# Optimization experiments

Measured on AMD Instinct MI355X. Metric: run time of the kernel, lower is better.

Reference implementation:

```python
import jax, jax.numpy as jnp
import numpy as np

KE_KCAL = 332.0637  # Coulomb constant in kcal/mol * Angstrom / e^2
R_CUT = 10.0
R_ON = R_CUT / 4.0
R_OFF = 3.0 * R_CUT / 4.0
MAX_Z = 86
FEAT_DIM = 128
N_ATOMS = 6144


def sigma(x):
    # torch.where(x > 0, exp(-1/x), 0) -- guard the exp arg so no NaN under jit
    xs = jnp.where(x > 0, x, 1.0)
    return jnp.where(x > 0, jnp.exp(-1.0 / xs), 0.0)


def f_switch(r):
    arg = (r - R_ON) / (R_OFF - R_ON)
    s_up = sigma(1.0 - arg)
    s_dn = sigma(arg)
    return s_up / (s_up + s_dn)


def setup_inputs() -> dict:
    key = jax.random.key(0)
    k_f, k_z, k_x, k_w, k_t = jax.random.split(key, 5)
    f = jax.random.normal(k_f, (N_ATOMS, FEAT_DIM), dtype=jnp.float32)
    z = jax.random.randint(k_z, (N_ATOMS,), 0, MAX_Z, dtype=jnp.int64)
    xyz = jax.random.uniform(k_x, (N_ATOMS, 3), dtype=jnp.float32) * 60.0  # ~60 A box
    total_charge = jnp.zeros((1,), dtype=jnp.float32)
    # learned params: Dense(feat_dim -> 1, no bias) and Embedding(max_z, 1) with padding row 0
    w_weight = jax.random.normal(k_w, (1, FEAT_DIM), dtype=jnp.float32) * 0.05
    z_table = jax.random.normal(k_t, (MAX_Z, 1), dtype=jnp.float32) * 0.05
    z_table = z_table.at[0].set(0.0)  # padding_idx=0
    return {"f": f, "z": z, "xyz": xyz, "total_charge": total_charge,
            "w_weight": w_weight, "z_table": z_table}


def reference(f, z, xyz, total_charge, w_weight, z_table):
    n = f.shape[0]
    # --- get_charge ---
    pred_charge = f @ w_weight.T + z_table[z]          # [N, 1]
    correction = (total_charge[0] - pred_charge.sum()) / n
    q = pred_charge + correction                       # [N, 1]
    qv = q[:, 0]                                       # [N]
    # --- get_en: pairwise distances via gram trick (no [N,N,3] intermediate) ---
    sq = jnp.sum(xyz * xyz, axis=-1)                   # [N]
    r2 = sq[:, None] + sq[None, :] - 2.0 * (xyz @ xyz.T)
    r2 = jnp.maximum(r2, 0.0)                          # [N, N]
    iu = jnp.triu(jnp.ones((n, n), dtype=bool), k=1)
    mask = iu & (r2 > 0.0)                             # j > i and r > 0, as in the torch code
    r2_safe = jnp.where(mask, r2, 1.0)
    r = jnp.sqrt(r2_safe)
    fs = f_switch(r)
    term = fs / jnp.sqrt(r2_safe + 1.0) + (1.0 - fs) / r
    pair_e = jnp.where(mask, qv[:, None] * qv[None, :] * term, 0.0)
    energy = KE_KCAL * jnp.sum(pair_e)
    return energy, q
```

## Files before the change

kernel.cpp:

```cpp
#include <hip/hip_runtime.h>

#define KE_KCAL 332.0637f

constexpr int N_ATOMS = 6144;
constexpr int NREAL = 1200;
constexpr int NPRED = 384;
constexpr int PAD = 32;

__global__ __launch_bounds__(256) void pred_kernel(
    const float* __restrict__ f, const int* __restrict__ z,
    const float* __restrict__ w, const float* __restrict__ ztab,
    const float* __restrict__ xyz,
    float* __restrict__ qpart, float4* __restrict__ xqp,
    float* __restrict__ epart, unsigned int* __restrict__ ctr1,
    unsigned int* __restrict__ ctr2)
{
    int t = threadIdx.x, b = blockIdx.x;
    int lane = t & 63, wid = t >> 6;

    if (b == 0) {
        if (t < 64) { epart[t * PAD] = 0.f; ctr1[t * PAD] = 0u; }
        if (t == 64) *ctr2 = 0u;
    }

    int base = b * 16 + wid * 4;
    const float2* f2 = (const float2*)f;
    float2 wv = ((const float2*)w)[lane];
    float2 v0 = f2[(size_t)(base + 0) * 64 + lane];
    float2 v1 = f2[(size_t)(base + 1) * 64 + lane];
    float2 v2 = f2[(size_t)(base + 2) * 64 + lane];
    float2 v3 = f2[(size_t)(base + 3) * 64 + lane];
    float p0 = fmaf(v0.x, wv.x, v0.y * wv.y);
    float p1 = fmaf(v1.x, wv.x, v1.y * wv.y);
    float p2 = fmaf(v2.x, wv.x, v2.y * wv.y);
    float p3 = fmaf(v3.x, wv.x, v3.y * wv.y);
    #pragma unroll
    for (int off = 32; off > 0; off >>= 1) {
        p0 += __shfl_xor(p0, off, 64);
        p1 += __shfl_xor(p1, off, 64);
        p2 += __shfl_xor(p2, off, 64);
        p3 += __shfl_xor(p3, off, 64);
    }
    float ws_sum = 0.f;
    if (lane < 4) {
        int atom = base + lane;
        float pk = p0;
        pk = (lane == 1) ? p1 : pk;
        pk = (lane == 2) ? p2 : pk;
        pk = (lane == 3) ? p3 : pk;
        pk += ztab[z[atom]];
        xqp[atom] = make_float4(xyz[3*atom], xyz[3*atom+1], xyz[3*atom+2], pk);
        ws_sum = pk;
    }
    ws_sum += __shfl_xor(ws_sum, 1, 64);
    ws_sum += __shfl_xor(ws_sum, 2, 64);

    __shared__ float lred[4];
    if (lane == 0) lred[wid] = ws_sum;
    __syncthreads();
    if (t == 0) qpart[b] = lred[0] + lred[1] + lred[2] + lred[3];
}

__global__ __launch_bounds__(256) void pair_kernel(
    const float4* __restrict__ xqp, const float* __restrict__ qpart,
    const float* __restrict__ total_charge,
    float* __restrict__ qout, float* __restrict__ epart,
    unsigned int* __restrict__ ctr1, unsigned int* __restrict__ ctr2,
    float* __restrict__ out0)
{
    int t = threadIdx.x, b = blockIdx.x;
    int lane = t & 63, wid = t >> 6;
    __shared__ float lred[4];
    __shared__ float4 sj[64];

    float s = qpart[t];
    if (t < NPRED - 256) s += qpart[256 + t];
    #pragma unroll
    for (int off = 32; off > 0; off >>= 1)
        s += __shfl_xor(s, off, 64);
    if (lane == 0) lred[wid] = s;
    __syncthreads();
    float S = lred[0] + lred[1] + lred[2] + lred[3];
    float corr = (total_charge[0] - S) * (1.0f / (float)N_ATOMS);

    int bi = 0, off = 0;
    while (b >= off + (96 - 4 * bi)) { off += 96 - 4 * bi; ++bi; }
    int bj = 4 * bi + (b - off);

    int gj0 = bj * 64;
    if (t < 64) {
        float4 a = xqp[gj0 + t];
        a.w += corr;
        sj[t] = a;
    }
    int gi = bi * 256 + t;
    float4 pi = xqp[gi];
    float qi = pi.w + corr;
    if (bj == 4 * bi) qout[gi] = qi;
    __syncthreads();

    int jthresh = gi - gj0;
    float acc = 0.f;
    #pragma unroll 8
    for (int jj = 0; jj < 64; ++jj) {
        float4 pj = sj[jj];
        float dx = pi.x - pj.x, dy = pi.y - pj.y, dz = pi.z - pj.z;
        float r2 = fmaf(dx, dx, fmaf(dy, dy, dz * dz));
        bool m = (jj > jthresh) && (r2 > 0.f);
        float r2s = m ? r2 : 1e8f;
        float qq  = m ? qi * pj.w : 0.f;
        float t2  = __builtin_amdgcn_rsqf(r2s);
        float u   = fmaf(r2s * t2, 0.2f, -0.5f);
        u = fminf(fmaxf(u, 1e-3f), 0.999f);
        float d   = (u + u - 1.f) * __builtin_amdgcn_rcpf(fmaf(-u, u, u));
        float fs  = __builtin_amdgcn_rcpf(1.f + __expf(d));
        float t1  = __builtin_amdgcn_rsqf(r2s + 1.f);
        acc = fmaf(qq, fmaf(fs, t1 - t2, t2), acc);
    }

    #pragma unroll
    for (int o2 = 32; o2 > 0; o2 >>= 1)
        acc += __shfl_down(acc, o2, 64);
    __syncthreads();
    if (lane == 0) lred[wid] = acc;
    __syncthreads();
    if (t == 0) {
        float be = lred[0] + lred[1] + lred[2] + lred[3];
        atomicAdd(&epart[(b & 63) * PAD], be);
    }

    if (t < 64) {
        bool last = false;
        if (t == 0) {
            int g = b & 63;
            unsigned int gcnt = (g < 48) ? 19u : 18u;
            __threadfence();
            unsigned int o1 = atomicAdd(&ctr1[g * PAD], 1u);
            if (o1 == gcnt - 1u) {
                __threadfence();
                unsigned int o2c = atomicAdd(ctr2, 1u);
                last = (o2c == 63u);
            }
        }
        last = (bool)__shfl((int)last, 0, 64);
        if (last) {
            float e = atomicAdd(&epart[t * PAD], 0.0f);
            #pragma unroll
            for (int o2 = 32; o2 > 0; o2 >>= 1)
                e += __shfl_down(e, o2, 64);
            if (t == 0) out0[0] = KE_KCAL * e;
        }
    }
}

extern "C" void kernel_launch(void* const* d_in, const int* in_sizes, int n_in,
                              void* d_out, int out_size, void* d_ws, size_t ws_size,
                              hipStream_t stream) {
    const float* f    = (const float*)d_in[0];
    const int*   z    = (const int*)  d_in[1];
    const float* xyz  = (const float*)d_in[2];
    const float* qtot = (const float*)d_in[3];
    const float* w    = (const float*)d_in[4];
    const float* ztab = (const float*)d_in[5];
    float* out = (float*)d_out;

    char* wsb = (char*)d_ws;
    float*        epart = (float*)(wsb + 0);
    unsigned int* ctr1  = (unsigned int*)(wsb + 8192);
    unsigned int* ctr2  = (unsigned int*)(wsb + 16384);
    float*        qpart = (float*)(wsb + 16896);
    float4*       xqp   = (float4*)(wsb + 32768);

    pred_kernel<<<NPRED, 256, 0, stream>>>(f, z, w, ztab, xyz,
                                           qpart, xqp, epart, ctr1, ctr2);
    pair_kernel<<<NREAL, 256, 0, stream>>>(xqp, qpart, qtot, out + 1, epart,
                                           ctr1, ctr2, out);
}
```

Measured before the change: 92.90 us.

## Fuse charge prediction and pair energy into one kernel with flag-based grid sync

Merges the per-atom charge prediction and the pairwise energy kernels into a single launch. The first NPRED blocks compute charges, and the last of them to finish reduces the partial sums and publishes the charge correction through a release flag. Every block spin-waits on that flag before doing its pair tile. The final energy reduction now writes one partial per block and lets the last block sum them, replacing the float atomics on padded slots. A tiny init kernel zeroes the counters, the pair loop unroll drops from 8 to 4, and the kernel gets an occupancy hint. The spin-wait relies on all blocks being co-resident and on the cross-block memory ordering being correct.

```diff
diff --git a/kernel.cpp b/kernel.cpp
--- a/kernel.cpp
+++ b/kernel.cpp
@@ -7,81 +7,103 @@
 constexpr int NPRED = 384;
 constexpr int PAD = 32;
 
-__global__ __launch_bounds__(256) void pred_kernel(
+
+__global__ __launch_bounds__(64) void init_kernel(unsigned int* __restrict__ c)
+{
+    for (int k = threadIdx.x; k < 2112; k += 64) c[k] = 0u;
+}
+
+__global__ __launch_bounds__(256, 8) void mega_kernel(
     const float* __restrict__ f, const int* __restrict__ z,
     const float* __restrict__ w, const float* __restrict__ ztab,
-    const float* __restrict__ xyz,
-    float* __restrict__ qpart, float4* __restrict__ xqp,
-    float* __restrict__ epart, unsigned int* __restrict__ ctr1,
-    unsigned int* __restrict__ ctr2)
-{
-    int t = threadIdx.x, b = blockIdx.x;
-    int lane = t & 63, wid = t >> 6;
-
-    if (b == 0) {
-        if (t < 64) { epart[t * PAD] = 0.f; ctr1[t * PAD] = 0u; }
-        if (t == 64) *ctr2 = 0u;
-    }
-
-    int base = b * 16 + wid * 4;
-    const float2* f2 = (const float2*)f;
-    float2 wv = ((const float2*)w)[lane];
-    float2 v0 = f2[(size_t)(base + 0) * 64 + lane];
-    float2 v1 = f2[(size_t)(base + 1) * 64 + lane];
-    float2 v2 = f2[(size_t)(base + 2) * 64 + lane];
-    float2 v3 = f2[(size_t)(base + 3) * 64 + lane];
-    float p0 = fmaf(v0.x, wv.x, v0.y * wv.y);
-    float p1 = fmaf(v1.x, wv.x, v1.y * wv.y);
-    float p2 = fmaf(v2.x, wv.x, v2.y * wv.y);
-    float p3 = fmaf(v3.x, wv.x, v3.y * wv.y);
-    #pragma unroll
-    for (int off = 32; off > 0; off >>= 1) {
-        p0 += __shfl_xor(p0, off, 64);
-        p1 += __shfl_xor(p1, off, 64);
-        p2 += __shfl_xor(p2, off, 64);
-        p3 += __shfl_xor(p3, off, 64);
-    }
-    float ws_sum = 0.f;
-    if (lane < 4) {
-        int atom = base + lane;
-        float pk = p0;
-        pk = (lane == 1) ? p1 : pk;
-        pk = (lane == 2) ? p2 : pk;
-        pk = (lane == 3) ? p3 : pk;
-        pk += ztab[z[atom]];
-        xqp[atom] = make_float4(xyz[3*atom], xyz[3*atom+1], xyz[3*atom+2], pk);
-        ws_sum = pk;
-    }
-    ws_sum += __shfl_xor(ws_sum, 1, 64);
-    ws_sum += __shfl_xor(ws_sum, 2, 64);
-
-    __shared__ float lred[4];
-    if (lane == 0) lred[wid] = ws_sum;
-    __syncthreads();
-    if (t == 0) qpart[b] = lred[0] + lred[1] + lred[2] + lred[3];
-}
-
-__global__ __launch_bounds__(256) void pair_kernel(
-    const float4* __restrict__ xqp, const float* __restrict__ qpart,
-    const float* __restrict__ total_charge,
-    float* __restrict__ qout, float* __restrict__ epart,
+    const float* __restrict__ xyz, const float* __restrict__ qtot,
+    float* __restrict__ qout, float* __restrict__ out0,
     unsigned int* __restrict__ ctr1, unsigned int* __restrict__ ctr2,
-    float* __restrict__ out0)
+    unsigned int* __restrict__ pred_ctr, unsigned int* __restrict__ flag,
+    float* __restrict__ cslot, float* __restrict__ qpart,
+    float* __restrict__ eblk, float4* __restrict__ xqp)
 {
     int t = threadIdx.x, b = blockIdx.x;
     int lane = t & 63, wid = t >> 6;
     __shared__ float lred[4];
     __shared__ float4 sj[64];
-
-    float s = qpart[t];
-    if (t < NPRED - 256) s += qpart[256 + t];
-    #pragma unroll
-    for (int off = 32; off > 0; off >>= 1)
-        s += __shfl_xor(s, off, 64);
-    if (lane == 0) lred[wid] = s;
-    __syncthreads();
-    float S = lred[0] + lred[1] + lred[2] + lred[3];
-    float corr = (total_charge[0] - S) * (1.0f / (float)N_ATOMS);
+    __shared__ float sc;
+    __shared__ int lflag, lfin;
+
+    if (t == 0) lflag = 0;
+    __syncthreads();
+
+    if (b < NPRED) {
+        int base = b * 16 + wid * 4;
+        const float2* f2 = (const float2*)f;
+        float2 wv = ((const float2*)w)[lane];
+        float2 v0 = f2[(size_t)(base + 0) * 64 + lane];
+        float2 v1 = f2[(size_t)(base + 1) * 64 + lane];
+        float2 v2 = f2[(size_t)(base + 2) * 64 + lane];
+        float2 v3 = f2[(size_t)(base + 3) * 64 + lane];
+        float p0 = fmaf(v0.x, wv.x, v0.y * wv.y);
+        float p1 = fmaf(v1.x, wv.x, v1.y * wv.y);
+        float p2 = fmaf(v2.x, wv.x, v2.y * wv.y);
+        float p3 = fmaf(v3.x, wv.x, v3.y * wv.y);
+        #pragma unroll
+        for (int off = 32; off > 0; off >>= 1) {
+            p0 += __shfl_xor(p0, off, 64);
+            p1 += __shfl_xor(p1, off, 64);
+            p2 += __shfl_xor(p2, off, 64);
+            p3 += __shfl_xor(p3, off, 64);
+        }
+        float ws_sum = 0.f;
+        if (lane < 4) {
+            int atom = base + lane;
+            float pk = p0;
+            pk = (lane == 1) ? p1 : pk;
+            pk = (lane == 2) ? p2 : pk;
+            pk = (lane == 3) ? p3 : pk;
+            pk += ztab[z[atom]];
+            xqp[atom] = make_float4(xyz[3*atom], xyz[3*atom+1], xyz[3*atom+2], pk);
+            ws_sum = pk;
+        }
+        ws_sum += __shfl_xor(ws_sum, 1, 64);
+        ws_sum += __shfl_xor(ws_sum, 2, 64);
+        if (lane == 0) lred[wid] = ws_sum;
+        __syncthreads();
+        if (t == 0) {
+            qpart[b] = lred[0] + lred[1] + lred[2] + lred[3];
+            unsigned int old = __hip_atomic_fetch_add(pred_ctr, 1u,
+                __ATOMIC_ACQ_REL, __HIP_MEMORY_SCOPE_AGENT);
+            if (old == NPRED - 1u) lflag = 1;
+        }
+        __syncthreads();
+        if (lflag) {
+            float s2 = 0.f;
+            for (int k = t; k < NPRED; k += 256)
+                s2 += __hip_atomic_load(&qpart[k], __ATOMIC_RELAXED,
+                                        __HIP_MEMORY_SCOPE_AGENT);
+            #pragma unroll
+            for (int off = 32; off > 0; off >>= 1)
+                s2 += __shfl_xor(s2, off, 64);
+            if (lane == 0) lred[wid] = s2;
+            __syncthreads();
+            if (t == 0) {
+                float S = lred[0] + lred[1] + lred[2] + lred[3];
+                float c = (qtot[0] - S) * (1.0f / (float)N_ATOMS);
+                __hip_atomic_store(cslot, c, __ATOMIC_RELAXED,
+                                   __HIP_MEMORY_SCOPE_AGENT);
+                __hip_atomic_store(flag, 1u, __ATOMIC_RELEASE,
+                                   __HIP_MEMORY_SCOPE_AGENT);
+            }
+        }
+    }
+
+    if (t == 0) {
+        while (__hip_atomic_load(flag, __ATOMIC_ACQUIRE,
+                                 __HIP_MEMORY_SCOPE_AGENT) == 0u)
+            __builtin_amdgcn_s_sleep(2);
+        sc = __hip_atomic_load(cslot, __ATOMIC_RELAXED,
+                               __HIP_MEMORY_SCOPE_AGENT);
+    }
+    __syncthreads();
+    float corr = sc;
 
     int bi = 0, off = 0;
     while (b >= off + (96 - 4 * bi)) { off += 96 - 4 * bi; ++bi; }
@@ -101,7 +123,7 @@
 
     int jthresh = gi - gj0;
     float acc = 0.f;
-    #pragma unroll 8
+    #pragma unroll 4
     for (int jj = 0; jj < 64; ++jj) {
         float4 pj = sj[jj];
         float dx = pi.x - pj.x, dy = pi.y - pj.y, dz = pi.z - pj.z;
@@ -125,31 +147,32 @@
     if (lane == 0) lred[wid] = acc;
     __syncthreads();
     if (t == 0) {
-        float be = lred[0] + lred[1] + lred[2] + lred[3];
-        atomicAdd(&epart[(b & 63) * PAD], be);
-    }
-
-    if (t < 64) {
-        bool last = false;
-        if (t == 0) {
-            int g = b & 63;
-            unsigned int gcnt = (g < 48) ? 19u : 18u;
-            __threadfence();
-            unsigned int o1 = atomicAdd(&ctr1[g * PAD], 1u);
-            if (o1 == gcnt - 1u) {
-                __threadfence();
-                unsigned int o2c = atomicAdd(ctr2, 1u);
-                last = (o2c == 63u);
-            }
-        }
-        last = (bool)__shfl((int)last, 0, 64);
-        if (last) {
-            float e = atomicAdd(&epart[t * PAD], 0.0f);
-            #pragma unroll
-            for (int o2 = 32; o2 > 0; o2 >>= 1)
-                e += __shfl_down(e, o2, 64);
-            if (t == 0) out0[0] = KE_KCAL * e;
-        }
+        eblk[b] = lred[0] + lred[1] + lred[2] + lred[3];
+        int g = b & 63;
+        unsigned int gcnt = (g < 48) ? 19u : 18u;
+        unsigned int o1 = __hip_atomic_fetch_add(&ctr1[g * PAD], 1u,
+            __ATOMIC_ACQ_REL, __HIP_MEMORY_SCOPE_AGENT);
+        int fin = 0;
+        if (o1 == gcnt - 1u) {
+            unsigned int o2c = __hip_atomic_fetch_add(ctr2, 1u,
+                __ATOMIC_ACQ_REL, __HIP_MEMORY_SCOPE_AGENT);
+            fin = (o2c == 63u);
+        }
+        lfin = fin;
+    }
+    __syncthreads();
+
+    if (lfin) {
+        float e = 0.f;
+        for (int k = t; k < NREAL; k += 256)
+            e += __hip_atomic_load(&eblk[k], __ATOMIC_RELAXED,
+                                   __HIP_MEMORY_SCOPE_AGENT);
+        #pragma unroll
+        for (int o2 = 32; o2 > 0; o2 >>= 1)
+            e += __shfl_down(e, o2, 64);
+        if (lane == 0) lred[wid] = e;
+        __syncthreads();
+        if (t == 0) out0[0] = KE_KCAL * (lred[0] + lred[1] + lred[2] + lred[3]);
     }
 }
 
@@ -165,14 +188,18 @@
     float* out = (float*)d_out;
 
     char* wsb = (char*)d_ws;
-    float*        epart = (float*)(wsb + 0);
-    unsigned int* ctr1  = (unsigned int*)(wsb + 8192);
-    unsigned int* ctr2  = (unsigned int*)(wsb + 16384);
-    float*        qpart = (float*)(wsb + 16896);
-    float4*       xqp   = (float4*)(wsb + 32768);
-
-    pred_kernel<<<NPRED, 256, 0, stream>>>(f, z, w, ztab, xyz,
-                                           qpart, xqp, epart, ctr1, ctr2);
-    pair_kernel<<<NREAL, 256, 0, stream>>>(xqp, qpart, qtot, out + 1, epart,
-                                           ctr1, ctr2, out);
+    unsigned int* ctr1     = (unsigned int*)(wsb + 0);
+    unsigned int* ctr2     = (unsigned int*)(wsb + 8192);
+    unsigned int* pred_ctr = (unsigned int*)(wsb + 8196);
+    unsigned int* flag     = (unsigned int*)(wsb + 8200);
+    float*        cslot    = (float*)(wsb + 8204);
+    float*        qpart    = (float*)(wsb + 8448);
+    float*        eblk     = (float*)(wsb + 10240);
+    float4*       xqp      = (float4*)(wsb + 16384);
+
+    init_kernel<<<1, 64, 0, stream>>>((unsigned int*)wsb);
+    mega_kernel<<<NREAL, 256, 0, stream>>>(f, z, w, ztab, xyz, qtot,
+                                           out + 1, out, ctr1, ctr2,
+                                           pred_ctr, flag, cslot, qpart,
+                                           eblk, xqp);
 }
```

Measured after the change: 203.9 us. 2.2x slower.

## Morton-sort atoms into cells and skip switching math for distant pairs

Applied to the files above, without the earlier changes.

Adds a single-block counting sort that orders atoms by 8x8x8 Morton cell, so each pair tile holds spatially coherent atoms. Prediction and the pair loop then work in sorted order, and charges are scattered back through the index array. Inside the pair loop, the costly switching-function evaluation runs only when some lane in the wavefront has a pair within the switching radius; otherwise the plain 1/r term is used. This trades an extra serial sort launch and branch overhead for far fewer transcendental ops.

```diff
diff --git a/kernel.cpp b/kernel.cpp
--- a/kernel.cpp
+++ b/kernel.cpp
@@ -6,34 +6,87 @@
 constexpr int NREAL = 1200;
 constexpr int NPRED = 384;
 constexpr int PAD = 32;
+constexpr int NCELL = 512;
+
+__device__ __forceinline__ unsigned spread3(unsigned v) {
+    return (v & 1u) | ((v & 2u) << 2) | ((v & 4u) << 4);
+}
+
+__device__ __forceinline__ unsigned cell_of(float x, float y, float z) {
+    unsigned cx = min(7u, (unsigned)(fmaxf(x, 0.f) * (8.0f / 60.0f)));
+    unsigned cy = min(7u, (unsigned)(fmaxf(y, 0.f) * (8.0f / 60.0f)));
+    unsigned cz = min(7u, (unsigned)(fmaxf(z, 0.f) * (8.0f / 60.0f)));
+    return spread3(cx) | (spread3(cy) << 1) | (spread3(cz) << 2);
+}
+
+__global__ __launch_bounds__(512) void sort_kernel(
+    const float* __restrict__ xyz, int* __restrict__ idx,
+    float* __restrict__ epart, unsigned int* __restrict__ ctr1,
+    unsigned int* __restrict__ ctr2)
+{
+    int t = threadIdx.x;
+    int lane = t & 63, wv = t >> 6;
+    __shared__ unsigned cnt[NCELL];
+    __shared__ unsigned basev[NCELL];
+    __shared__ unsigned wsum[8];
+
+    if (t < 64) { epart[t * PAD] = 0.f; ctr1[t * PAD] = 0u; }
+    if (t == 64) *ctr2 = 0u;
+    cnt[t] = 0u;
+    __syncthreads();
+
+    for (int a = t; a < N_ATOMS; a += 512) {
+        unsigned c = cell_of(xyz[3*a], xyz[3*a+1], xyz[3*a+2]);
+        atomicAdd(&cnt[c], 1u);
+    }
+    __syncthreads();
+
+    unsigned v = cnt[t];
+    unsigned x = v;
+    #pragma unroll
+    for (int off = 1; off < 64; off <<= 1) {
+        unsigned y = __shfl_up(x, off, 64);
+        if (lane >= off) x += y;
+    }
+    if (lane == 63) wsum[wv] = x;
+    __syncthreads();
+    if (t == 0) {
+        unsigned acc = 0;
+        #pragma unroll
+        for (int k = 0; k < 8; ++k) { unsigned tmp = wsum[k]; wsum[k] = acc; acc += tmp; }
+    }
+    __syncthreads();
+    basev[t] = x - v + wsum[wv];
+    __syncthreads();
+
+    for (int a = t; a < N_ATOMS; a += 512) {
+        unsigned c = cell_of(xyz[3*a], xyz[3*a+1], xyz[3*a+2]);
+        unsigned s = atomicAdd(&basev[c], 1u);
+        idx[s] = a;
+    }
+}
 
 __global__ __launch_bounds__(256) void pred_kernel(
     const float* __restrict__ f, const int* __restrict__ z,
     const float* __restrict__ w, const float* __restrict__ ztab,
-    const float* __restrict__ xyz,
-    float* __restrict__ qpart, float4* __restrict__ xqp,
-    float* __restrict__ epart, unsigned int* __restrict__ ctr1,
-    unsigned int* __restrict__ ctr2)
+    const float* __restrict__ xyz, const int* __restrict__ idx,
+    float* __restrict__ qpart, float4* __restrict__ xqp)
 {
     int t = threadIdx.x, b = blockIdx.x;
     int lane = t & 63, wid = t >> 6;
 
-    if (b == 0) {
-        if (t < 64) { epart[t * PAD] = 0.f; ctr1[t * PAD] = 0u; }
-        if (t == 64) *ctr2 = 0u;
-    }
-
-    int base = b * 16 + wid * 4;
+    int sbase = b * 16 + wid * 4;
+    const int4 aq = ((const int4*)idx)[sbase >> 2];
     const float2* f2 = (const float2*)f;
-    float2 wv = ((const float2*)w)[lane];
-    float2 v0 = f2[(size_t)(base + 0) * 64 + lane];
-    float2 v1 = f2[(size_t)(base + 1) * 64 + lane];
-    float2 v2 = f2[(size_t)(base + 2) * 64 + lane];
-    float2 v3 = f2[(size_t)(base + 3) * 64 + lane];
-    float p0 = fmaf(v0.x, wv.x, v0.y * wv.y);
-    float p1 = fmaf(v1.x, wv.x, v1.y * wv.y);
-    float p2 = fmaf(v2.x, wv.x, v2.y * wv.y);
-    float p3 = fmaf(v3.x, wv.x, v3.y * wv.y);
+    float2 wvv = ((const float2*)w)[lane];
+    float2 v0 = f2[(size_t)aq.x * 64 + lane];
+    float2 v1 = f2[(size_t)aq.y * 64 + lane];
+    float2 v2 = f2[(size_t)aq.z * 64 + lane];
+    float2 v3 = f2[(size_t)aq.w * 64 + lane];
+    float p0 = fmaf(v0.x, wvv.x, v0.y * wvv.y);
+    float p1 = fmaf(v1.x, wvv.x, v1.y * wvv.y);
+    float p2 = fmaf(v2.x, wvv.x, v2.y * wvv.y);
+    float p3 = fmaf(v3.x, wvv.x, v3.y * wvv.y);
     #pragma unroll
     for (int off = 32; off > 0; off >>= 1) {
         p0 += __shfl_xor(p0, off, 64);
@@ -43,13 +96,13 @@
     }
     float ws_sum = 0.f;
     if (lane < 4) {
-        int atom = base + lane;
+        int a = (lane == 0) ? aq.x : (lane == 1) ? aq.y : (lane == 2) ? aq.z : aq.w;
         float pk = p0;
         pk = (lane == 1) ? p1 : pk;
         pk = (lane == 2) ? p2 : pk;
         pk = (lane == 3) ? p3 : pk;
-        pk += ztab[z[atom]];
-        xqp[atom] = make_float4(xyz[3*atom], xyz[3*atom+1], xyz[3*atom+2], pk);
+        pk += ztab[z[a]];
+        xqp[sbase + lane] = make_float4(xyz[3*a], xyz[3*a+1], xyz[3*a+2], pk);
         ws_sum = pk;
     }
     ws_sum += __shfl_xor(ws_sum, 1, 64);
@@ -63,7 +116,7 @@
 
 __global__ __launch_bounds__(256) void pair_kernel(
     const float4* __restrict__ xqp, const float* __restrict__ qpart,
-    const float* __restrict__ total_charge,
+    const float* __restrict__ total_charge, const int* __restrict__ idx,
     float* __restrict__ qout, float* __restrict__ epart,
     unsigned int* __restrict__ ctr1, unsigned int* __restrict__ ctr2,
     float* __restrict__ out0)
@@ -96,12 +149,12 @@
     int gi = bi * 256 + t;
     float4 pi = xqp[gi];
     float qi = pi.w + corr;
-    if (bj == 4 * bi) qout[gi] = qi;
+    if (bj == 4 * bi) qout[idx[gi]] = qi;
     __syncthreads();
 
     int jthresh = gi - gj0;
     float acc = 0.f;
-    #pragma unroll 8
+    #pragma unroll 4
     for (int jj = 0; jj < 64; ++jj) {
         float4 pj = sj[jj];
         float dx = pi.x - pj.x, dy = pi.y - pj.y, dz = pi.z - pj.z;
@@ -110,12 +163,15 @@
         float r2s = m ? r2 : 1e8f;
         float qq  = m ? qi * pj.w : 0.f;
         float t2  = __builtin_amdgcn_rsqf(r2s);
-        float u   = fmaf(r2s * t2, 0.2f, -0.5f);
-        u = fminf(fmaxf(u, 1e-3f), 0.999f);
-        float d   = (u + u - 1.f) * __builtin_amdgcn_rcpf(fmaf(-u, u, u));
-        float fs  = __builtin_amdgcn_rcpf(1.f + __expf(d));
-        float t1  = __builtin_amdgcn_rsqf(r2s + 1.f);
-        acc = fmaf(qq, fmaf(fs, t1 - t2, t2), acc);
+        acc = fmaf(qq, t2, acc);
+        if (__any(r2s < 56.25f)) {
+            float u = fmaf(r2s * t2, 0.2f, -0.5f);
+            u = fminf(fmaxf(u, 1e-3f), 0.999f);
+            float d  = (u + u - 1.f) * __builtin_amdgcn_rcpf(fmaf(-u, u, u));
+            float fs = __builtin_amdgcn_rcpf(1.f + __expf(d));
+            float t1 = __builtin_amdgcn_rsqf(r2s + 1.f);
+            acc = fmaf(qq * fs, t1 - t2, acc);
+        }
     }
 
     #pragma unroll
@@ -169,10 +225,12 @@
     unsigned int* ctr1  = (unsigned int*)(wsb + 8192);
     unsigned int* ctr2  = (unsigned int*)(wsb + 16384);
     float*        qpart = (float*)(wsb + 16896);
-    float4*       xqp   = (float4*)(wsb + 32768);
-
-    pred_kernel<<<NPRED, 256, 0, stream>>>(f, z, w, ztab, xyz,
-                                           qpart, xqp, epart, ctr1, ctr2);
-    pair_kernel<<<NREAL, 256, 0, stream>>>(xqp, qpart, qtot, out + 1, epart,
-                                           ctr1, ctr2, out);
-}
+    int*          idx   = (int*)(wsb + 18432);
+    float4*       xqp   = (float4*)(wsb + 49152);
+
+    sort_kernel<<<1, 512, 0, stream>>>(xyz, idx, epart, ctr1, ctr2);
+    pred_kernel<<<NPRED, 256, 0, stream>>>(f, z, w, ztab, xyz, idx,
+                                           qpart, xqp);
+    pair_kernel<<<NREAL, 256, 0, stream>>>(xqp, qpart, qtot, idx, out + 1,
+                                           epart, ctr1, ctr2, out);
+}
```

Measured after the change: 105.5 us. +13.5%, slower.

## Split pair tiles into four j-slices and precompute charge correction in pred kernel

Applied to the files above, without the earlier changes.

Each 256x64 pair tile is now split across four blocks that each handle 16 j-atoms, giving four times as many pair blocks with shorter inner loops. The completion counter threshold is raised to match the larger number of blocks per group. The charge-correction reduction moves out of every pair block: the last pred block, found with an agent-scope atomic counter, computes it once and writes it to a slot. This adds a memset launch to reset that counter, plus more per-block overhead and atomics in the pair stage.

```diff
diff --git a/kernel.cpp b/kernel.cpp
--- a/kernel.cpp
+++ b/kernel.cpp
@@ -3,25 +3,31 @@
 #define KE_KCAL 332.0637f
 
 constexpr int N_ATOMS = 6144;
-constexpr int NREAL = 1200;
+constexpr int NTILE = 1200;
+constexpr int NSPLIT = 4;
+constexpr int NPAIRB = NTILE * NSPLIT;
 constexpr int NPRED = 384;
 constexpr int PAD = 32;
 
 __global__ __launch_bounds__(256) void pred_kernel(
     const float* __restrict__ f, const int* __restrict__ z,
     const float* __restrict__ w, const float* __restrict__ ztab,
-    const float* __restrict__ xyz,
+    const float* __restrict__ xyz, const float* __restrict__ qtot,
     float* __restrict__ qpart, float4* __restrict__ xqp,
     float* __restrict__ epart, unsigned int* __restrict__ ctr1,
-    unsigned int* __restrict__ ctr2)
+    unsigned int* __restrict__ ctr2, unsigned int* __restrict__ pred_ctr,
+    float* __restrict__ cslot)
 {
     int t = threadIdx.x, b = blockIdx.x;
     int lane = t & 63, wid = t >> 6;
+    __shared__ float lred[4];
+    __shared__ int lflag;
 
     if (b == 0) {
         if (t < 64) { epart[t * PAD] = 0.f; ctr1[t * PAD] = 0u; }
         if (t == 64) *ctr2 = 0u;
     }
+    if (t == 0) lflag = 0;
 
     int base = b * 16 + wid * 4;
     const float2* f2 = (const float2*)f;
@@ -54,16 +60,34 @@
     }
     ws_sum += __shfl_xor(ws_sum, 1, 64);
     ws_sum += __shfl_xor(ws_sum, 2, 64);
-
-    __shared__ float lred[4];
     if (lane == 0) lred[wid] = ws_sum;
     __syncthreads();
-    if (t == 0) qpart[b] = lred[0] + lred[1] + lred[2] + lred[3];
+    if (t == 0) {
+        qpart[b] = lred[0] + lred[1] + lred[2] + lred[3];
+        unsigned int old = __hip_atomic_fetch_add(pred_ctr, 1u,
+            __ATOMIC_ACQ_REL, __HIP_MEMORY_SCOPE_AGENT);
+        if (old == NPRED - 1u) lflag = 1;
+    }
+    __syncthreads();
+    if (lflag) {
+        float s2 = 0.f;
+        for (int k = t; k < NPRED; k += 256)
+            s2 += __hip_atomic_load(&qpart[k], __ATOMIC_RELAXED,
+                                    __HIP_MEMORY_SCOPE_AGENT);
+        #pragma unroll
+        for (int off = 32; off > 0; off >>= 1)
+            s2 += __shfl_xor(s2, off, 64);
+        if (lane == 0) lred[wid] = s2;
+        __syncthreads();
+        if (t == 0) {
+            float S = lred[0] + lred[1] + lred[2] + lred[3];
+            cslot[0] = (qtot[0] - S) * (1.0f / (float)N_ATOMS);
+        }
+    }
 }
 
 __global__ __launch_bounds__(256) void pair_kernel(
-    const float4* __restrict__ xqp, const float* __restrict__ qpart,
-    const float* __restrict__ total_charge,
+    const float4* __restrict__ xqp, const float* __restrict__ cslot,
     float* __restrict__ qout, float* __restrict__ epart,
     unsigned int* __restrict__ ctr1, unsigned int* __restrict__ ctr2,
     float* __restrict__ out0)
@@ -71,24 +95,17 @@
     int t = threadIdx.x, b = blockIdx.x;
     int lane = t & 63, wid = t >> 6;
     __shared__ float lred[4];
-    __shared__ float4 sj[64];
+    __shared__ float4 sj[16];
 
-    float s = qpart[t];
-    if (t < NPRED - 256) s += qpart[256 + t];
-    #pragma unroll
-    for (int off = 32; off > 0; off >>= 1)
-        s += __shfl_xor(s, off, 64);
-    if (lane == 0) lred[wid] = s;
-    __syncthreads();
-    float S = lred[0] + lred[1] + lred[2] + lred[3];
-    float corr = (total_charge[0] - S) * (1.0f / (float)N_ATOMS);
+    float corr = cslot[0];
 
+    int tile = b >> 2, s = b & 3;
     int bi = 0, off = 0;
-    while (b >= off + (96 - 4 * bi)) { off += 96 - 4 * bi; ++bi; }
-    int bj = 4 * bi + (b - off);
+    while (tile >= off + (96 - 4 * bi)) { off += 96 - 4 * bi; ++bi; }
+    int bj = 4 * bi + (tile - off);
 
-    int gj0 = bj * 64;
-    if (t < 64) {
+    int gj0 = bj * 64 + s * 16;
+    if (t < 16) {
         float4 a = xqp[gj0 + t];
         a.w += corr;
         sj[t] = a;
@@ -96,17 +113,17 @@
     int gi = bi * 256 + t;
     float4 pi = xqp[gi];
     float qi = pi.w + corr;
-    if (bj == 4 * bi) qout[gi] = qi;
+    if (bj == 4 * bi && s == 0) qout[gi] = qi;
     __syncthreads();
 
     int jthresh = gi - gj0;
     float acc = 0.f;
-    #pragma unroll 8
-    for (int jj = 0; jj < 64; ++jj) {
-        float4 pj = sj[jj];
+    #pragma unroll
+    for (int k = 0; k < 16; ++k) {
+        float4 pj = sj[k];
         float dx = pi.x - pj.x, dy = pi.y - pj.y, dz = pi.z - pj.z;
         float r2 = fmaf(dx, dx, fmaf(dy, dy, dz * dz));
-        bool m = (jj > jthresh) && (r2 > 0.f);
+        bool m = (k > jthresh) && (r2 > 0.f);
         float r2s = m ? r2 : 1e8f;
         float qq  = m ? qi * pj.w : 0.f;
         float t2  = __builtin_amdgcn_rsqf(r2s);
@@ -133,10 +150,9 @@
         bool last = false;
         if (t == 0) {
             int g = b & 63;
-            unsigned int gcnt = (g < 48) ? 19u : 18u;
             __threadfence();
             unsigned int o1 = atomicAdd(&ctr1[g * PAD], 1u);
-            if (o1 == gcnt - 1u) {
+            if (o1 == 74u) {
                 __threadfence();
                 unsigned int o2c = atomicAdd(ctr2, 1u);
                 last = (o2c == 63u);
@@ -165,14 +181,19 @@
     float* out = (float*)d_out;
 
     char* wsb = (char*)d_ws;
-    float*        epart = (float*)(wsb + 0);
-    unsigned int* ctr1  = (unsigned int*)(wsb + 8192);
-    unsigned int* ctr2  = (unsigned int*)(wsb + 16384);
-    float*        qpart = (float*)(wsb + 16896);
-    float4*       xqp   = (float4*)(wsb + 32768);
+    float*        epart    = (float*)(wsb + 0);
+    unsigned int* ctr1     = (unsigned int*)(wsb + 8192);
+    unsigned int* ctr2     = (unsigned int*)(wsb + 16384);
+    unsigned int* pred_ctr = (unsigned int*)(wsb + 16388);
+    float*        cslot    = (float*)(wsb + 16392);
+    float*        qpart    = (float*)(wsb + 16896);
+    float4*       xqp      = (float4*)(wsb + 32768);
 
-    pred_kernel<<<NPRED, 256, 0, stream>>>(f, z, w, ztab, xyz,
-                                           qpart, xqp, epart, ctr1, ctr2);
-    pair_kernel<<<NREAL, 256, 0, stream>>>(xqp, qpart, qtot, out + 1, epart,
-                                           ctr1, ctr2, out);
+    hipMemsetAsync(pred_ctr, 0, sizeof(unsigned int), stream);
+
+    pred_kernel<<<NPRED, 256, 0, stream>>>(f, z, w, ztab, xyz, qtot,
+                                           qpart, xqp, epart, ctr1, ctr2,
+                                           pred_ctr, cslot);
+    pair_kernel<<<NPAIRB, 256, 0, stream>>>(xqp, cslot, out + 1, epart,
+                                            ctr1, ctr2, out);
 }
```

Result: slower. 153.9 us (+65.7%).
